# Optimization experiments

Hardware: AMD Instinct MI355X
Metric: run time of the kernel (lower is better)

## Reference

```python
import jax, jax.numpy as jnp
import numpy as np

WSZ = 8
HEADS = 8
FILTER_RATE = 0.3
EPS = 1e-5


def layer_norm(x, w, b):
    mu = x.mean(-1, keepdims=True)
    var = ((x - mu) ** 2).mean(-1, keepdims=True)
    return (x - mu) * jax.lax.rsqrt(var + EPS) * w + b


def setup_inputs() -> dict:
    key = jax.random.key(0)
    ks = jax.random.split(key, 8)
    B, C, H, W = 2, 256, 512, 512
    C2 = 2 * C
    s = 0.02
    return {
        "feature_map": jax.random.normal(ks[0], (B, C, H, W), jnp.float32),
        "uncertain_map": jax.random.uniform(ks[1], (B, H, W), jnp.float32),
        "norm_w": jnp.ones((C,), jnp.float32),
        "norm_b": jnp.zeros((C,), jnp.float32),
        "lin0_w": jax.random.normal(ks[2], (C, C2), jnp.float32) * s,
        "lin0_b": jnp.zeros((C2,), jnp.float32),
        "qkv0_w": jax.random.normal(ks[3], (C2, 3 * C2), jnp.float32) * s,
        "lin1_w": jax.random.normal(ks[4], (C2, C2), jnp.float32) * s,
        "lin1_b": jnp.zeros((C2,), jnp.float32),
        "qkv1_w": jax.random.normal(ks[5], (C2, 3 * C2), jnp.float32) * s,
        "proj_w": jax.random.normal(ks[6], (C2, C), jnp.float32) * s,
        "proj_b": jnp.zeros((C,), jnp.float32),
    }


def _window_attn(xf, qkv_w, scale, winsz, C2):
    # xf: (N, winsz, C2)
    qkv = (xf @ qkv_w).reshape(-1, winsz, 3, HEADS, C2 // HEADS)
    q, k, v = qkv[:, :, 0], qkv[:, :, 1], qkv[:, :, 2]  # (N, winsz, H, dh)
    a = jnp.einsum("nqhd,nkhd->nhqk", q, k) * scale
    a = jax.nn.softmax(a, axis=-1)
    o = jnp.einsum("nhqk,nkhd->nqhd", a, v).reshape(-1, winsz, C2)
    return xf + o


def reference(feature_map, uncertain_map, norm_w, norm_b, lin0_w, lin0_b,
              qkv0_w, lin1_w, lin1_b, qkv1_w, proj_w, proj_b):
    B, C, H, W = feature_map.shape
    wsz = WSZ
    nH, nW = H // wsz, W // wsz
    nWin, winsz = nH * nW, wsz * wsz
    nWF = int(nWin * FILTER_RATE)
    C2 = 2 * C
    scale = (C // HEADS) ** -0.5  # module uses C//num_heads, not C2//num_heads

    # window partition
    x = jnp.transpose(feature_map, (0, 2, 3, 1))  # B H W C
    win_x = x.reshape(B, nH, wsz, nW, wsz, C).transpose(0, 1, 3, 2, 4, 5)
    win_x = win_x.reshape(B * nWin, winsz, C)
    win_unc = uncertain_map.reshape(B, nH, wsz, nW, wsz).transpose(0, 1, 3, 2, 4)
    win_unc = win_unc.reshape(B, nWin, winsz)

    # topk window selection by mean uncertainty
    score = win_unc.mean(-1)  # (B, nWin)
    _, idx = jax.lax.top_k(score, nWF)  # (B, nWF)
    flat_idx = (idx + jnp.arange(B)[:, None] * nWin).reshape(-1)  # (B*nWF,)

    xw = win_x[flat_idx]  # gather: (B*nWF, winsz, C)
    xn = layer_norm(xw, norm_w, norm_b)

    # local branch: repeat 0
    xf = jax.nn.gelu(xn @ lin0_w + lin0_b, approximate=False)
    xf = _window_attn(xf, qkv0_w, scale, winsz, C2)
    # repeat 1
    xf = xf + jax.nn.gelu(xf @ lin1_w + lin1_b, approximate=False)
    xf = _window_attn(xf, qkv1_w, scale, winsz, C2)

    out_f = xn + jax.nn.gelu(xf @ proj_w + proj_b, approximate=False)

    # scatter-add back into unnormalized windows
    win_x = win_x.at[flat_idx].add(out_f)

    x = win_x.reshape(B, nH, nW, wsz, wsz, C).transpose(0, 1, 3, 2, 4, 5)
    x = x.reshape(B, H, W, C)
    return jnp.transpose(x, (0, 3, 1, 2))
```

## Files before the change

### kernel.cpp

```cpp
#include <hip/hip_runtime.h>
#include <math.h>

typedef unsigned short u16;
typedef unsigned int   u32;
typedef __attribute__((ext_vector_type(8))) short bf16x8;
typedef __attribute__((ext_vector_type(4))) float f32x4;

#define DEV static __device__ __forceinline__

DEV u16 f2b(float f) {
  union { float f; u32 u; } v; v.f = f;
  u32 r = v.u + 0x7FFFu + ((v.u >> 16) & 1u);
  return (u16)(r >> 16);
}
DEV float b2f(u16 h) {
  union { u32 u; float f; } v; v.u = ((u32)h) << 16;
  return v.f;
}
DEV float gelu_f(float x) { return 0.5f * x * (1.0f + erff(x * 0.70710678118654752f)); }

DEV void gload16(const u16* g, u16* l) {
  __builtin_amdgcn_global_load_lds(
      (const __attribute__((address_space(1))) void*)g,
      (__attribute__((address_space(3))) void*)l, 16, 0, 0);
}

__global__ void k_transpose_w(const float* __restrict__ src, u16* __restrict__ dst,
                              int K, int N) {
  long t = (long)blockIdx.x * 256 + threadIdx.x;
  if (t >= (long)K * N) return;
  int n = (int)(t / K), k = (int)(t % K);
  dst[t] = f2b(src[(long)k * N + n]);
}

__global__ void k_scores(const float* __restrict__ unc, float* __restrict__ scores) {
  int id = blockIdx.x * 256 + threadIdx.x;
  if (id >= 8192) return;
  int b = id >> 12, win = id & 4095;
  int h0 = (win >> 6) << 3, w0 = (win & 63) << 3;
  float r[8] = {0.f,0.f,0.f,0.f,0.f,0.f,0.f,0.f};
  for (int i = 0; i < 8; ++i) {
    long base = ((long)(b * 512 + h0 + i)) * 512 + w0;
    #pragma unroll
    for (int j = 0; j < 8; ++j) r[j] += unc[base + j];
  }
  float s = ((r[0] + r[1]) + (r[2] + r[3])) + ((r[4] + r[5]) + (r[6] + r[7]));
  scores[id] = s * (1.0f / 64.0f);
}

__global__ __launch_bounds__(1024) void k_topk(
    const float* __restrict__ scores, int* __restrict__ row2win,
    int* __restrict__ win2row, int nWF) {
  __shared__ float ls[4096];
  __shared__ int   li[4096];
  const int b = blockIdx.x;
  const int tid = threadIdx.x;
  for (int i = tid; i < 4096; i += 1024) {
    ls[i] = scores[b * 4096 + i];
    li[i] = i;
    win2row[b * 4096 + i] = -1;
  }
  __syncthreads();
  for (int k = 2; k <= 4096; k <<= 1) {
    for (int j = k >> 1; j > 0; j >>= 1) {
      for (int t = tid; t < 2048; t += 1024) {
        int i = ((t / j) * (j << 1)) + (t % j);
        int ixj = i + j;
        bool up = ((i & k) == 0);
        float sa = ls[i], sb = ls[ixj];
        int ia = li[i], ib = li[ixj];
        bool g = (sa > sb) || (sa == sb && ia < ib);
        if (g != up) { ls[i] = sb; ls[ixj] = sa; li[i] = ib; li[ixj] = ia; }
      }
      __syncthreads();
    }
  }
  for (int r = tid; r < nWF; r += 1024) {
    int win = li[r];
    row2win[b * nWF + r] = (b << 12) | win;
    win2row[b * 4096 + win] = b * nWF + r;
  }
}

__global__ __launch_bounds__(256) void k_gather_ln(
    const float* __restrict__ fm, const float* __restrict__ nw,
    const float* __restrict__ nb, const int* __restrict__ row2win,
    u16* __restrict__ xn, int winStart) {
  __shared__ float sx[64 * 256];
  const int tid = threadIdx.x;
  const int rw = row2win[winStart + blockIdx.x];
  const int b = rw >> 12, win = rw & 4095;
  const int h0 = (win >> 6) << 3, w0 = (win & 63) << 3;
  {
    const int c = tid;
    long base = ((long)(b * 256 + c) * 512 + h0) * 512 + w0;
    for (int i = 0; i < 8; ++i) {
      float4 v0 = *(const float4*)(fm + base + (long)i * 512);
      float4 v1 = *(const float4*)(fm + base + (long)i * 512 + 4);
      float vv[8] = {v0.x, v0.y, v0.z, v0.w, v1.x, v1.y, v1.z, v1.w};
      #pragma unroll
      for (int j = 0; j < 8; ++j) {
        int tok = i * 8 + j;
        sx[tok * 256 + (c ^ ((tok & 15) << 1))] = vv[j];
      }
    }
  }
  __syncthreads();
  const int tok = tid >> 2, g = tid & 3;
  const int swz = (tok & 15) << 1;
  float sum = 0.f;
  for (int q = 0; q < 64; ++q) sum += sx[tok * 256 + ((g * 64 + q) ^ swz)];
  sum += __shfl_xor(sum, 1);
  sum += __shfl_xor(sum, 2);
  const float mu = sum * (1.0f / 256.0f);
  float s2 = 0.f;
  for (int q = 0; q < 64; ++q) {
    float d = sx[tok * 256 + ((g * 64 + q) ^ swz)] - mu;
    s2 += d * d;
  }
  s2 += __shfl_xor(s2, 1);
  s2 += __shfl_xor(s2, 2);
  const float rs = rsqrtf(s2 * (1.0f / 256.0f) + 1e-5f);
  long obase = ((long)blockIdx.x * 64 + tok) * 256 + g * 64;
  for (int q8 = 0; q8 < 8; ++q8) {
    u16 tmp[8];
    #pragma unroll
    for (int e = 0; e < 8; ++e) {
      int c = g * 64 + q8 * 8 + e;
      float v = (sx[tok * 256 + (c ^ swz)] - mu) * rs * nw[c] + nb[c];
      tmp[e] = f2b(v);
    }
    *(ulonglong2*)(xn + obase + q8 * 8) = *(const ulonglong2*)tmp;
  }
}

template <int EPI, int NT>
__global__ __launch_bounds__(512, 2) void k_gemm256(
    const u16* __restrict__ A, const u16* __restrict__ Bt,
    const float* __restrict__ bias, const u16* __restrict__ Res,
    u16* __restrict__ Y, int N, int K) {
  __shared__ __attribute__((aligned(16))) u16 S[65536];
  const int tid = threadIdx.x;
  const int l = tid & 63, wid = tid >> 6;
  const int wm = wid >> 2, wn = wid & 3;

  const int nwg = gridDim.x;
  const int d = blockIdx.x;
  const int xcd = d & 7, j = d >> 3;
  const int q = nwg >> 3, r8 = nwg & 7;
  const int wrk = (xcd < r8 ? xcd * (q + 1) : r8 * (q + 1) + (xcd - r8) * q) + j;
  const int tm = wrk / NT, tn = wrk % NT;

  const int srow = wid * 8 + (l >> 3);
  const int k0b = ((l & 7) << 4) ^ ((l >> 3) << 4);
  const u16* gA = A + (long)(tm * 256 + srow) * K + (k0b >> 1);
  const u16* gB = Bt + (long)(tn * 256 + srow) * K + (k0b >> 1);
  char* ldsS = (char*)S + wid * 1024 + l * 16;
  const char* Sb = (const char*)S;

  f32x4 acc[8][4] = {};
  bf16x8 bfrag[4][2];
  bf16x8 af[2][2];

#define STG(T, ISB, H) do { \
    const u16* g_ = (ISB) ? gB : gA; \
    char* lp_ = ldsS + ((T) & 1) * 65536 + (ISB) * 32768 + (H) * 16384; \
    gload16(g_ + (long)((H) * 128) * K + (long)(T) * 64, (u16*)lp_); \
    gload16(g_ + (long)((H) * 128 + 64) * K + (long)(T) * 64, (u16*)(lp_ + 8192)); \
  } while (0)

#define DS_B(T) do { \
    _Pragma("unroll") for (int ni_ = 0; ni_ < 4; ++ni_) { \
      const int r_ = wn * 64 + ni_ * 16 + (l & 15); \
      _Pragma("unroll") for (int kk_ = 0; kk_ < 2; ++kk_) { \
        const int kb_ = kk_ * 64 + ((l >> 4) << 4); \
        bfrag[ni_][kk_] = *(const bf16x8*)(Sb + ((T) & 1) * 65536 + 32768 + r_ * 128 + (kb_ ^ ((r_ & 7) << 4))); \
      } } \
  } while (0)

#define DS_A(T, Q) do { \
    _Pragma("unroll") for (int m2_ = 0; m2_ < 2; ++m2_) { \
      const int r_ = wm * 128 + (2 * (Q) + m2_) * 16 + (l & 15); \
      _Pragma("unroll") for (int kk_ = 0; kk_ < 2; ++kk_) { \
        const int kb_ = kk_ * 64 + ((l >> 4) << 4); \
        af[m2_][kk_] = *(const bf16x8*)(Sb + ((T) & 1) * 65536 + r_ * 128 + (kb_ ^ ((r_ & 7) << 4))); \
      } } \
  } while (0)

#define MFMA16(Q) do { \
    _Pragma("unroll") for (int m2_ = 0; m2_ < 2; ++m2_) \
      _Pragma("unroll") for (int ni_ = 0; ni_ < 4; ++ni_) \
        _Pragma("unroll") for (int kk_ = 0; kk_ < 2; ++kk_) \
          acc[2 * (Q) + m2_][ni_] = __builtin_amdgcn_mfma_f32_16x16x32_bf16( \
              af[m2_][kk_], bfrag[ni_][kk_], acc[2 * (Q) + m2_][ni_], 0, 0, 0); \
  } while (0)

#define BAR_MFMA(Q) do { \
    __builtin_amdgcn_s_barrier(); \
    asm volatile("s_waitcnt lgkmcnt(0)" ::: "memory"); \
    __builtin_amdgcn_sched_barrier(0); \
    __builtin_amdgcn_s_setprio(1); \
    MFMA16(Q); \
    __builtin_amdgcn_s_setprio(0); \
  } while (0)

#define PH_END() do { \
    __builtin_amdgcn_s_barrier(); \
    __builtin_amdgcn_sched_barrier(0); \
  } while (0)

  STG(0, 0, 0); STG(0, 0, 1); STG(0, 1, 0); STG(0, 1, 1);
  STG(1, 0, 0); STG(1, 0, 1); STG(1, 1, 0); STG(1, 1, 1);
  asm volatile("s_waitcnt vmcnt(8)" ::: "memory");
  __builtin_amdgcn_s_barrier();
  __builtin_amdgcn_sched_barrier(0);

  const int nIter = K >> 7;
  for (int i = 0; i < nIter; ++i) {
    const int t0 = 2 * i, t1 = 2 * i + 1;
    const bool more = (i + 1 < nIter);
    DS_B(t0); DS_A(t0, 0);
    if (i > 0) STG(t1, 0, 0);
    BAR_MFMA(0); PH_END();
    DS_A(t0, 1);
    if (i > 0) STG(t1, 0, 1);
    if (more) STG(t0 + 2, 1, 0);
    BAR_MFMA(1); PH_END();
    DS_A(t0, 2);
    if (more) STG(t0 + 2, 1, 1);
    BAR_MFMA(2); PH_END();
    DS_A(t0, 3);
    BAR_MFMA(3);
    if (more) { asm volatile("s_waitcnt vmcnt(4)" ::: "memory"); }
    else      { asm volatile("s_waitcnt vmcnt(0)" ::: "memory"); }
    PH_END();
    DS_B(t1); DS_A(t1, 0);
    if (more) STG(t0 + 2, 0, 0);
    BAR_MFMA(0); PH_END();
    DS_A(t1, 1);
    if (more) STG(t0 + 2, 0, 1);
    BAR_MFMA(1); PH_END();
    DS_A(t1, 2);
    if (more) STG(t1 + 2, 1, 0);
    BAR_MFMA(2); PH_END();
    DS_A(t1, 3);
    if (more) STG(t1 + 2, 1, 1);
    BAR_MFMA(3);
    if (more) { asm volatile("s_waitcnt vmcnt(4)" ::: "memory"); }
    PH_END();
  }

  float bv[4];
  if (EPI >= 1) {
    #pragma unroll
    for (int ni = 0; ni < 4; ++ni)
      bv[ni] = bias[tn * 256 + wn * 64 + ni * 16 + (l & 15)];
  }
  const long rbase = (long)tm * 256 + wm * 128 + ((l >> 4) << 2);
  const int cbase = tn * 256 + wn * 64 + (l & 15);
  #pragma unroll
  for (int mi = 0; mi < 8; ++mi) {
    #pragma unroll
    for (int r = 0; r < 4; ++r) {
      long m = rbase + mi * 16 + r;
      #pragma unroll
      for (int ni = 0; ni < 4; ++ni) {
        int n = cbase + ni * 16;
        float v = acc[mi][ni][r];
        if (EPI >= 1) v = gelu_f(v + bv[ni]);
        if (EPI >= 2) v += b2f(Res[m * N + n]);
        if (EPI == 3) {
          Y[((m >> 6) * 256 + n) * 64 + (m & 63)] = f2b(v);
        } else {
          Y[m * N + n] = f2b(v);
        }
      }
    }
  }
#undef STG
#undef DS_B
#undef DS_A
#undef MFMA16
#undef BAR_MFMA
#undef PH_END
}

__global__ __launch_bounds__(256) void k_attn(
    const u16* __restrict__ qkv, u16* __restrict__ xf) {
  __shared__ __attribute__((aligned(16))) u16 sq[64 * 64];
  __shared__ __attribute__((aligned(16))) u16 sk[64 * 64];
  __shared__ __attribute__((aligned(16))) u16 sv[64 * 64];
  __shared__ __attribute__((aligned(16))) u16 sp[64 * 64];
  const int tid = threadIdx.x;
  const int l = tid & 63, w = tid >> 6;
  const int wloc = blockIdx.x >> 3, h = blockIdx.x & 7;
  const long tokbase = (long)wloc * 64;

  #pragma unroll
  for (int cc = 0; cc < 2; ++cc) {
    int cid = tid * 2 + cc;
    int t = cid >> 3, d0 = (cid & 7) << 3;
    long gq = (tokbase + t) * 1536 + h * 64 + d0;
    ulonglong2 vq = *(const ulonglong2*)(qkv + gq);
    ulonglong2 vk = *(const ulonglong2*)(qkv + gq + 512);
    int sbyte = t * 128 + ((d0 * 2) ^ ((t & 7) << 4));
    *(ulonglong2*)((char*)sq + sbyte) = vq;
    *(ulonglong2*)((char*)sk + sbyte) = vk;
    u16 vv[8];
    *(ulonglong2*)vv = *(const ulonglong2*)(qkv + gq + 1024);
    #pragma unroll
    for (int e = 0; e < 8; ++e) {
      int r = d0 + e;
      *(u16*)((char*)sv + r * 128 + ((t * 2) ^ ((r & 7) << 4))) = vv[e];
    }
  }
  __syncthreads();

  f32x4 accs[4] = {};
  #pragma unroll
  for (int ks = 0; ks < 2; ++ks) {
    int kb = ks * 64 + ((l >> 4) << 4);
    int ra = w * 16 + (l & 15);
    bf16x8 aq = *(const bf16x8*)((char*)sq + ra * 128 + (kb ^ ((ra & 7) << 4)));
    #pragma unroll
    for (int cf = 0; cf < 4; ++cf) {
      int rb = cf * 16 + (l & 15);
      bf16x8 bk = *(const bf16x8*)((char*)sk + rb * 128 + (kb ^ ((rb & 7) << 4)));
      accs[cf] = __builtin_amdgcn_mfma_f32_16x16x32_bf16(aq, bk, accs[cf], 0, 0, 0);
    }
  }
  const float scale = 0.17677669529663687f;
  float pv[4][4];
  #pragma unroll
  for (int r = 0; r < 4; ++r) {
    float m = -1e30f;
    #pragma unroll
    for (int cf = 0; cf < 4; ++cf) {
      pv[cf][r] = accs[cf][r] * scale;
      m = fmaxf(m, pv[cf][r]);
    }
    for (int off = 1; off < 16; off <<= 1) m = fmaxf(m, __shfl_xor(m, off));
    float s = 0.f;
    #pragma unroll
    for (int cf = 0; cf < 4; ++cf) { pv[cf][r] = __expf(pv[cf][r] - m); s += pv[cf][r]; }
    for (int off = 1; off < 16; off <<= 1) s += __shfl_xor(s, off);
    float inv = 1.0f / s;
    #pragma unroll
    for (int cf = 0; cf < 4; ++cf) pv[cf][r] *= inv;
  }
  #pragma unroll
  for (int cf = 0; cf < 4; ++cf)
    #pragma unroll
    for (int r = 0; r < 4; ++r) {
      int pr = w * 16 + ((l >> 4) << 2) + r, pc = cf * 16 + (l & 15);
      *(u16*)((char*)sp + pr * 128 + ((pc * 2) ^ ((pr & 7) << 4))) = f2b(pv[cf][r]);
    }
  __syncthreads();

  f32x4 acco[4] = {};
  #pragma unroll
  for (int ks = 0; ks < 2; ++ks) {
    int kb = ks * 64 + ((l >> 4) << 4);
    int ra = w * 16 + (l & 15);
    bf16x8 ap = *(const bf16x8*)((char*)sp + ra * 128 + (kb ^ ((ra & 7) << 4)));
    #pragma unroll
    for (int cf = 0; cf < 4; ++cf) {
      int rb = cf * 16 + (l & 15);
      bf16x8 bvv = *(const bf16x8*)((char*)sv + rb * 128 + (kb ^ ((rb & 7) << 4)));
      acco[cf] = __builtin_amdgcn_mfma_f32_16x16x32_bf16(ap, bvv, acco[cf], 0, 0, 0);
    }
  }
  #pragma unroll
  for (int cf = 0; cf < 4; ++cf)
    #pragma unroll
    for (int r = 0; r < 4; ++r) {
      long m = tokbase + w * 16 + ((l >> 4) << 2) + r;
      int n = h * 64 + cf * 16 + (l & 15);
      long idx = m * 512 + n;
      xf[idx] = f2b(acco[cf][r] + b2f(xf[idx]));
    }
}

__global__ __launch_bounds__(256) void k_assemble(
    const float* __restrict__ fm, const u16* __restrict__ out_f,
    const int* __restrict__ win2row, float* __restrict__ out) {
  const int tid = threadIdx.x;
  const int bq = blockIdx.x;
  const int hw = bq & 63, c = (bq >> 6) & 255, b = bq >> 14;
  const int w0 = (tid & 127) << 2;
  const int hlo = tid >> 7;
  const int win = hw * 64 + (w0 >> 3);
  const int r = win2row[b * 4096 + win];
  const u16* ofb = out_f + ((long)(r < 0 ? 0 : r) * 256 + c) * 64 + (w0 & 7);
  const long base = ((long)(b * 256 + c) * 512 + hw * 8) * 512 + w0;
  #pragma unroll
  for (int jj = 0; jj < 4; ++jj) {
    const int h = jj * 2 + hlo;
    float4 v = *(const float4*)(fm + base + (long)h * 512);
    if (r >= 0) {
      ushort4 ov = *(const ushort4*)(ofb + h * 8);
      v.x += b2f(ov.x);
      v.y += b2f(ov.y);
      v.z += b2f(ov.z);
      v.w += b2f(ov.w);
    }
    *(float4*)(out + base + (long)h * 512) = v;
  }
}

extern "C" void kernel_launch(void* const* d_in, const int* in_sizes, int n_in,
                              void* d_out, int out_size, void* d_ws, size_t ws_size,
                              hipStream_t stream) {
  const float* fm     = (const float*)d_in[0];
  const float* unc    = (const float*)d_in[1];
  const float* nw     = (const float*)d_in[2];
  const float* nb     = (const float*)d_in[3];
  const float* w_lin0 = (const float*)d_in[4];
  const float* b_lin0 = (const float*)d_in[5];
  const float* w_qkv0 = (const float*)d_in[6];
  const float* w_lin1 = (const float*)d_in[7];
  const float* b_lin1 = (const float*)d_in[8];
  const float* w_qkv1 = (const float*)d_in[9];
  const float* w_proj = (const float*)d_in[10];
  const float* b_proj = (const float*)d_in[11];
  float* out = (float*)d_out;

  const int nWF = 1228, totWin = 2456;
  const long totTok = (long)totWin * 64;

  char* p = (char*)d_ws;
  auto alloc = [&](size_t bytes) {
    char* r = p;
    p += (bytes + 255) & ~(size_t)255;
    return r;
  };
  float* scores = (float*)alloc(8192 * 4);
  int* win2row  = (int*)alloc(8192 * 4);
  int* row2win  = (int*)alloc(totWin * 4);
  u16* wT       = (u16*)alloc((size_t)2097152 * 2);
  u16* out_f    = (u16*)alloc((size_t)(totTok + 256) * 256 * 2);
  size_t persist = (size_t)(p - (char*)d_ws);

  int wpc = totWin;
  {
    const int cands[6] = {1, 2, 4, 8, 16, 32};
    for (int ci = 0; ci < 6; ++ci) {
      int n = cands[ci];
      int wp = ((totWin + n - 1) / n + 3) & ~3;
      size_t mc = (size_t)wp * 64;
      size_t need = persist + 4096 +
                    ((mc * 256 * 2 + 255) & ~(size_t)255) +
                    2 * ((mc * 512 * 2 + 255) & ~(size_t)255) +
                    ((mc * 1536 * 2 + 255) & ~(size_t)255);
      if (need <= ws_size) { wpc = wp; break; }
    }
  }
  long mcap = (long)wpc * 64;
  u16* xn   = (u16*)alloc((size_t)mcap * 256 * 2);
  u16* xfa  = (u16*)alloc((size_t)mcap * 512 * 2);
  u16* xfb  = (u16*)alloc((size_t)mcap * 512 * 2);
  u16* qkvb = (u16*)alloc((size_t)mcap * 1536 * 2);

  u16* wT_lin0 = wT;
  u16* wT_qkv0 = wT + 131072;
  u16* wT_lin1 = wT + 917504;
  u16* wT_qkv1 = wT + 1179648;
  u16* wT_proj = wT + 1966080;
  k_transpose_w<<<(131072 + 255) / 256, 256, 0, stream>>>(w_lin0, wT_lin0, 256, 512);
  k_transpose_w<<<(786432 + 255) / 256, 256, 0, stream>>>(w_qkv0, wT_qkv0, 512, 1536);
  k_transpose_w<<<(262144 + 255) / 256, 256, 0, stream>>>(w_lin1, wT_lin1, 512, 512);
  k_transpose_w<<<(786432 + 255) / 256, 256, 0, stream>>>(w_qkv1, wT_qkv1, 512, 1536);
  k_transpose_w<<<(131072 + 255) / 256, 256, 0, stream>>>(w_proj, wT_proj, 512, 256);

  k_scores<<<32, 256, 0, stream>>>(unc, scores);
  k_topk<<<2, 1024, 0, stream>>>(scores, row2win, win2row, nWF);

  for (int w0 = 0; w0 < totWin; w0 += wpc) {
    int rem = totWin - w0;
    int wn = (wpc < rem) ? wpc : rem;
    int mT = wn / 4;
    k_gather_ln<<<wn, 256, 0, stream>>>(fm, nw, nb, row2win, xn, w0);
    k_gemm256<1, 2><<<mT * 2, 512, 0, stream>>>(xn, wT_lin0, b_lin0, nullptr, xfa, 512, 256);
    k_gemm256<0, 6><<<mT * 6, 512, 0, stream>>>(xfa, wT_qkv0, nullptr, nullptr, qkvb, 1536, 512);
    k_attn<<<wn * 8, 256, 0, stream>>>(qkvb, xfa);
    k_gemm256<2, 2><<<mT * 2, 512, 0, stream>>>(xfa, wT_lin1, b_lin1, xfa, xfb, 512, 512);
    k_gemm256<0, 6><<<mT * 6, 512, 0, stream>>>(xfb, wT_qkv1, nullptr, nullptr, qkvb, 1536, 512);
    k_attn<<<wn * 8, 256, 0, stream>>>(qkvb, xfb);
    k_gemm256<3, 1><<<mT * 1, 512, 0, stream>>>(xfb, wT_proj, b_proj, xn,
                                                out_f + (long)w0 * 16384, 256, 512);
  }
  k_assemble<<<32768, 256, 0, stream>>>(fm, out_f, win2row, out);
}
```

Before: 2.105 ms.

## Make GEMM persistent with cross-tile prefetch pipeline and reorder gather loads

```diff
diff --git a/kernel.cpp b/kernel.cpp
--- a/kernel.cpp
+++ b/kernel.cpp
@@ -92,15 +92,17 @@
   const int b = rw >> 12, win = rw & 4095;
   const int h0 = (win >> 6) << 3, w0 = (win & 63) << 3;
   {
-    const int c = tid;
-    long base = ((long)(b * 256 + c) * 512 + h0) * 512 + w0;
-    for (int i = 0; i < 8; ++i) {
-      float4 v0 = *(const float4*)(fm + base + (long)i * 512);
-      float4 v1 = *(const float4*)(fm + base + (long)i * 512 + 4);
+    const int c8 = tid >> 3, h = tid & 7;
+    #pragma unroll
+    for (int cc = 0; cc < 8; ++cc) {
+      const int c = cc * 32 + c8;
+      long base = ((long)(b * 256 + c) * 512 + h0 + h) * 512 + w0;
+      float4 v0 = *(const float4*)(fm + base);
+      float4 v1 = *(const float4*)(fm + base + 4);
       float vv[8] = {v0.x, v0.y, v0.z, v0.w, v1.x, v1.y, v1.z, v1.w};
       #pragma unroll
       for (int j = 0; j < 8; ++j) {
-        int tok = i * 8 + j;
+        int tok = h * 8 + j;
         sx[tok * 256 + (c ^ ((tok & 15) << 1))] = vv[j];
       }
     }
@@ -134,27 +136,29 @@
   }
 }
 
-template <int EPI, int NT>
+template <int EPI, int NT, int KD>
 __global__ __launch_bounds__(512, 2) void k_gemm256(
     const u16* __restrict__ A, const u16* __restrict__ Bt,
     const float* __restrict__ bias, const u16* __restrict__ Res,
-    u16* __restrict__ Y, int N, int K) {
+    u16* __restrict__ Y, int N, int nWork) {
+  constexpr int NKT = KD / 64;
+  constexpr int LG_NKT = (KD == 512) ? 3 : 2;
+  constexpr int NIP = KD / 128;
+  constexpr int LG_NIP = (KD == 512) ? 2 : 1;
   __shared__ __attribute__((aligned(16))) u16 S[65536];
   const int tid = threadIdx.x;
   const int l = tid & 63, wid = tid >> 6;
   const int wm = wid >> 2, wn = wid & 3;
 
-  const int nwg = gridDim.x;
-  const int d = blockIdx.x;
-  const int xcd = d & 7, j = d >> 3;
-  const int q = nwg >> 3, r8 = nwg & 7;
-  const int wrk = (xcd < r8 ? xcd * (q + 1) : r8 * (q + 1) + (xcd - r8) * q) + j;
-  const int tm = wrk / NT, tn = wrk % NT;
+  const int slot = ((blockIdx.x & 7) << 5) | (blockIdx.x >> 3);
+  const int q = nWork >> 8, rr = nWork & 255;
+  const int wrkBase = slot * q + (slot < rr ? slot : rr);
+  const int myN = q + (slot < rr ? 1 : 0);
+  if (myN == 0) return;
 
   const int srow = wid * 8 + (l >> 3);
   const int k0b = ((l & 7) << 4) ^ ((l >> 3) << 4);
-  const u16* gA = A + (long)(tm * 256 + srow) * K + (k0b >> 1);
-  const u16* gB = Bt + (long)(tn * 256 + srow) * K + (k0b >> 1);
+  const int vko = k0b >> 1;
   char* ldsS = (char*)S + wid * 1024 + l * 16;
   const char* Sb = (const char*)S;
 
@@ -162,11 +166,16 @@
   bf16x8 bfrag[4][2];
   bf16x8 af[2][2];
 
-#define STG(T, ISB, H) do { \
-    const u16* g_ = (ISB) ? gB : gA; \
-    char* lp_ = ldsS + ((T) & 1) * 65536 + (ISB) * 32768 + (H) * 16384; \
-    gload16(g_ + (long)((H) * 128) * K + (long)(T) * 64, (u16*)lp_); \
-    gload16(g_ + (long)((H) * 128 + 64) * K + (long)(T) * 64, (u16*)(lp_ + 8192)); \
+#define STG(G, ISB, H) do { \
+    const int wig_ = (G) >> LG_NKT; \
+    const int ktg_ = (G) & (NKT - 1); \
+    const int wrkg_ = wrkBase + wig_; \
+    const int tmg_ = wrkg_ / NT, tng_ = wrkg_ % NT; \
+    const u16* g_ = (ISB) ? Bt + (long)(tng_ * 256 + srow) * KD + vko \
+                          : A + (long)(tmg_ * 256 + srow) * KD + vko; \
+    char* lp_ = ldsS + ((G) & 1) * 65536 + (ISB) * 32768 + (H) * 16384; \
+    gload16(g_ + (long)((H) * 128) * KD + ktg_ * 64, (u16*)lp_); \
+    gload16(g_ + (long)((H) * 128 + 64) * KD + ktg_ * 64, (u16*)(lp_ + 8192)); \
   } while (0)
 
 #define DS_B(T) do { \
@@ -215,15 +224,15 @@
   __builtin_amdgcn_s_barrier();
   __builtin_amdgcn_sched_barrier(0);
 
-  const int nIter = K >> 7;
-  for (int i = 0; i < nIter; ++i) {
-    const int t0 = 2 * i, t1 = 2 * i + 1;
-    const bool more = (i + 1 < nIter);
+  const int giEnd = myN * NIP;
+  for (int gi = 0; gi < giEnd; ++gi) {
+    const int t0 = 2 * gi, t1 = t0 + 1;
+    const bool more = (gi + 1 < giEnd);
     DS_B(t0); DS_A(t0, 0);
-    if (i > 0) STG(t1, 0, 0);
+    if (gi > 0) STG(t1, 0, 0);
     BAR_MFMA(0); PH_END();
     DS_A(t0, 1);
-    if (i > 0) STG(t1, 0, 1);
+    if (gi > 0) STG(t1, 0, 1);
     if (more) STG(t0 + 2, 1, 0);
     BAR_MFMA(1); PH_END();
     DS_A(t0, 2);
@@ -248,33 +257,42 @@
     BAR_MFMA(3);
     if (more) { asm volatile("s_waitcnt vmcnt(4)" ::: "memory"); }
     PH_END();
-  }
-
-  float bv[4];
-  if (EPI >= 1) {
-    #pragma unroll
-    for (int ni = 0; ni < 4; ++ni)
-      bv[ni] = bias[tn * 256 + wn * 64 + ni * 16 + (l & 15)];
-  }
-  const long rbase = (long)tm * 256 + wm * 128 + ((l >> 4) << 2);
-  const int cbase = tn * 256 + wn * 64 + (l & 15);
-  #pragma unroll
-  for (int mi = 0; mi < 8; ++mi) {
-    #pragma unroll
-    for (int r = 0; r < 4; ++r) {
-      long m = rbase + mi * 16 + r;
+
+    if (((gi + 1) & (NIP - 1)) == 0) {
+      const int wrk = wrkBase + (gi >> LG_NIP);
+      const int tm = wrk / NT, tn = wrk % NT;
+      float bv[4];
+      if (EPI >= 1) {
+        #pragma unroll
+        for (int ni = 0; ni < 4; ++ni)
+          bv[ni] = bias[tn * 256 + wn * 64 + ni * 16 + (l & 15)];
+      }
+      const long rbase = (long)tm * 256 + wm * 128 + ((l >> 4) << 2);
+      const int cbase = tn * 256 + wn * 64 + (l & 15);
       #pragma unroll
-      for (int ni = 0; ni < 4; ++ni) {
-        int n = cbase + ni * 16;
-        float v = acc[mi][ni][r];
-        if (EPI >= 1) v = gelu_f(v + bv[ni]);
-        if (EPI >= 2) v += b2f(Res[m * N + n]);
-        if (EPI == 3) {
-          Y[((m >> 6) * 256 + n) * 64 + (m & 63)] = f2b(v);
-        } else {
-          Y[m * N + n] = f2b(v);
+      for (int mi = 0; mi < 8; ++mi) {
+        #pragma unroll
+        for (int r = 0; r < 4; ++r) {
+          long m = rbase + mi * 16 + r;
+          #pragma unroll
+          for (int ni = 0; ni < 4; ++ni) {
+            int n = cbase + ni * 16;
+            float v = acc[mi][ni][r];
+            if (EPI >= 1) v = gelu_f(v + bv[ni]);
+            if (EPI >= 2) v += b2f(Res[m * N + n]);
+            if (EPI == 3) {
+              Y[((m >> 6) * 256 + n) * 64 + (m & 63)] = f2b(v);
+            } else {
+              Y[m * N + n] = f2b(v);
+            }
+          }
         }
       }
+      #pragma unroll
+      for (int mi = 0; mi < 8; ++mi)
+        #pragma unroll
+        for (int ni = 0; ni < 4; ++ni)
+          acc[mi][ni] = (f32x4){0.f, 0.f, 0.f, 0.f};
     }
   }
 #undef STG
@@ -480,14 +498,14 @@
     int wn = (wpc < rem) ? wpc : rem;
     int mT = wn / 4;
     k_gather_ln<<<wn, 256, 0, stream>>>(fm, nw, nb, row2win, xn, w0);
-    k_gemm256<1, 2><<<mT * 2, 512, 0, stream>>>(xn, wT_lin0, b_lin0, nullptr, xfa, 512, 256);
-    k_gemm256<0, 6><<<mT * 6, 512, 0, stream>>>(xfa, wT_qkv0, nullptr, nullptr, qkvb, 1536, 512);
+    k_gemm256<1, 2, 256><<<256, 512, 0, stream>>>(xn, wT_lin0, b_lin0, nullptr, xfa, 512, mT * 2);
+    k_gemm256<0, 6, 512><<<256, 512, 0, stream>>>(xfa, wT_qkv0, nullptr, nullptr, qkvb, 1536, mT * 6);
     k_attn<<<wn * 8, 256, 0, stream>>>(qkvb, xfa);
-    k_gemm256<2, 2><<<mT * 2, 512, 0, stream>>>(xfa, wT_lin1, b_lin1, xfa, xfb, 512, 512);
-    k_gemm256<0, 6><<<mT * 6, 512, 0, stream>>>(xfb, wT_qkv1, nullptr, nullptr, qkvb, 1536, 512);
+    k_gemm256<2, 2, 512><<<256, 512, 0, stream>>>(xfa, wT_lin1, b_lin1, xfa, xfb, 512, mT * 2);
+    k_gemm256<0, 6, 512><<<256, 512, 0, stream>>>(xfb, wT_qkv1, nullptr, nullptr, qkvb, 1536, mT * 6);
     k_attn<<<wn * 8, 256, 0, stream>>>(qkvb, xfb);
-    k_gemm256<3, 1><<<mT * 1, 512, 0, stream>>>(xfb, wT_proj, b_proj, xn,
-                                                out_f + (long)w0 * 16384, 256, 512);
+    k_gemm256<3, 1, 512><<<256, 512, 0, stream>>>(xfb, wT_proj, b_proj, xn,
+                                                  out_f + (long)w0 * 16384, 256, mT * 1);
   }
   k_assemble<<<32768, 256, 0, stream>>>(fm, out_f, win2row, out);
 }
```

Result: faster. 2.033 ms (-3.4%).
